# Kernel tuning notes

Measured on AMD Instinct MI355X. Metric: run time of the kernel, lower is better.

Reference implementation:

```python
import jax, jax.numpy as jnp
import numpy as np

MODEL_DIM = 1024
HEAD_DIM = 64
NUM_HEADS = 16
FF_DIM = 4 * MODEL_DIM
ROT_DIM = 32  # max(head_dim // 2, 32)
FUSED = (NUM_HEADS * HEAD_DIM,) * 3 + (FF_DIM,) * 2
B, S = 2, 2048


def rotate_half(x):
    x1, x2 = jnp.split(x, 2, axis=-1)
    return jnp.concatenate([-x2, x1], axis=-1)


def rope_freqs(seq_len, dim=ROT_DIM, max_period=10000.0):
    inv_freq = 1.0 / max_period ** (jnp.arange(0, dim, 2, dtype=jnp.float32) / dim)
    freqs = jnp.arange(seq_len, dtype=jnp.float32)[:, None] * inv_freq[None, :]
    return jnp.concatenate([freqs, freqs], axis=-1)  # [S, dim]


def setup_inputs() -> dict:
    key = jax.random.key(0)
    ks = jax.random.split(key, 10)
    d = MODEL_DIM
    s_in = (sum(FUSED) ** -0.5)
    return {
        "inputs": jax.random.normal(ks[0], (B, S, d), jnp.float32),
        "time_embeds": jax.random.normal(ks[1], (B, 1, d), jnp.float32),
        "ln_w": jnp.ones((d,), jnp.float32),
        "ln_b": jnp.zeros((d,), jnp.float32),
        "cond_w": jax.random.normal(ks[2], (d, 2 * d), jnp.float32) * (d ** -0.5),
        "cond_b": jnp.zeros((2 * d,), jnp.float32),
        "w_in": jax.random.normal(ks[3], (d, sum(FUSED)), jnp.float32) * (d ** -0.5),
        "w_attn": jax.random.normal(ks[4], (NUM_HEADS * HEAD_DIM, d), jnp.float32) * ((NUM_HEADS * HEAD_DIM) ** -0.5),
        "w_ff": jax.random.normal(ks[5], (FF_DIM, d), jnp.float32) * (FF_DIM ** -0.5),
        "b_ff": jnp.zeros((d,), jnp.float32),
    }


def reference(inputs, time_embeds, ln_w, ln_b, cond_w, cond_b, w_in, w_attn, w_ff, b_ff):
    # LayerNorm
    mu = jnp.mean(inputs, axis=-1, keepdims=True)
    var = jnp.mean(jnp.square(inputs - mu), axis=-1, keepdims=True)
    units = (inputs - mu) * jax.lax.rsqrt(var + 1e-5) * ln_w + ln_b

    # FiLM conditioning
    cond = jax.nn.silu(time_embeds) @ cond_w + cond_b  # [B,1,2D]
    scale, bias = jnp.split(cond, 2, axis=-1)
    units = (1.0 + scale) * units + bias

    # Fused projection -> q, k, v, ff, ff_gate
    proj = units @ w_in
    splits = np.cumsum(FUSED)[:-1].tolist()
    q, k, v, ff, ff_gate = jnp.split(proj, splits, axis=-1)

    def split_heads(x):  # [B,S,H*hd] -> [B,H,S,hd]
        return x.reshape(B, S, NUM_HEADS, HEAD_DIM).transpose(0, 2, 1, 3)

    q, k, v = split_heads(q), split_heads(k), split_heads(v)

    # Rotary on first ROT_DIM dims of q, k
    freqs = rope_freqs(S)  # [S, ROT_DIM]
    cos, sin = jnp.cos(freqs), jnp.sin(freqs)

    def rope(x):
        xl, xr = x[..., :ROT_DIM], x[..., ROT_DIM:]
        xl = xl * cos + rotate_half(xl) * sin
        return jnp.concatenate([xl, xr], axis=-1)

    q, k = rope(q), rope(k)

    # Attention (full score matrix, manual softmax, as original)
    score = jnp.einsum("bhsd,bhSd->bhsS", q, k) * (HEAD_DIM ** -0.5)
    weight = jax.nn.softmax(score, axis=-1)
    attn = jnp.einsum("bhsS,bhSd->bhsd", weight, v)
    concat = attn.transpose(0, 2, 1, 3).reshape(B, S, NUM_HEADS * HEAD_DIM)
    attn_out = concat @ w_attn

    # GeGLU FF
    ff_out = (ff * jax.nn.gelu(ff_gate, approximate=True)) @ w_ff + b_ff

    return inputs + attn_out + ff_out
```

## Files before the change

### kernel.cpp

```cpp
#include <hip/hip_runtime.h>
#include <hip/hip_bf16.h>

typedef __attribute__((ext_vector_type(8))) __bf16 bf16x8;
typedef __attribute__((ext_vector_type(4))) float f32x4;
typedef unsigned short u16;
typedef unsigned int u32;

#define DMODEL 1024
#define SLEN   2048
#define NPROJ  11264
#define NFUSE  5120
#define MROWS  4096

__device__ __forceinline__ float b2f(u16 u){ u32 v=((u32)u)<<16; float f; __builtin_memcpy(&f,&v,4); return f; }
__device__ __forceinline__ u16 f2b(float f){ u32 u; __builtin_memcpy(&u,&f,4); u32 r=u+0x7fffu+((u>>16)&1u); return (u16)(r>>16); }
__device__ __forceinline__ float fexp2(float x){ return __builtin_amdgcn_exp2f(x); }

__device__ __forceinline__ void gload16(const void* g, void* l){
  __builtin_amdgcn_global_load_lds((__attribute__((address_space(1))) u32*)g,
                                   (__attribute__((address_space(3))) u32*)l, 16, 0, 0);
}

template<int REMAP>
__global__ __launch_bounds__(256) void k_transpose(const float* __restrict__ src, int N,
                                                   u16* __restrict__ dst, int ldd, int coloff){
  __shared__ float tile[32][33];
  int n0 = blockIdx.x*32, k0 = blockIdx.y*32;
  int tx = threadIdx.x & 31, ty = threadIdx.x >> 5;
  int srccol;
  if (REMAP && (n0 + tx) >= 3072){
    int c = n0 + tx - 3072;
    int q = c >> 5, o = c & 31;
    srccol = (o < 16) ? (3072 + 16*q + o) : (7168 + 16*q + (o-16));
  } else srccol = n0 + tx;
  #pragma unroll
  for (int r=0;r<4;r++)
    tile[ty*4+r][tx] = src[(size_t)(k0+ty*4+r)*N + srccol];
  __syncthreads();
  #pragma unroll
  for (int r=0;r<4;r++){
    int n = ty*4+r;
    dst[(size_t)(n0+n)*ldd + coloff + k0 + tx] = f2b(tile[tx][n]);
  }
}

__global__ __launch_bounds__(256) void k_rope_table(float* __restrict__ tab){
  int idx = blockIdx.x*256 + threadIdx.x;
  if (idx >= SLEN*16) return;
  int s = idx >> 4, i = idx & 15;
  float inv = powf(10000.f, -(float)i/16.f);
  float f = (float)s * inv;
  tab[s*32 + i]      = cosf(f);
  tab[s*32 + 16 + i] = sinf(f);
}

__global__ __launch_bounds__(256) void k_cond(const float* __restrict__ te, const float* __restrict__ cw,
                                              const float* __restrict__ cb, float* __restrict__ cond){
  __shared__ float sl[DMODEL];
  int b = blockIdx.y, t = threadIdx.x;
  for (int i=t;i<DMODEL;i+=256){ float x = te[b*DMODEL+i]; sl[i] = x/(1.f+expf(-x)); }
  __syncthreads();
  int n = blockIdx.x*256 + t;
  float acc = 0.f;
  for (int k=0;k<DMODEL;k++) acc += sl[k]*cw[(size_t)k*2048 + n];
  cond[b*2048+n] = acc + cb[n];
}

__global__ __launch_bounds__(256) void k_ln(const float* __restrict__ x, const float* __restrict__ lw,
                                            const float* __restrict__ lb, const float* __restrict__ cond,
                                            u16* __restrict__ units){
  int row = blockIdx.x; int b = row >> 11;
  int t = threadIdx.x;
  const float4 v = *(const float4*)(x + (size_t)row*DMODEL + t*4);
  float s = v.x+v.y+v.z+v.w;
  float q = v.x*v.x+v.y*v.y+v.z*v.z+v.w*v.w;
  #pragma unroll
  for (int off=32; off; off>>=1){ s += __shfl_xor(s,off); q += __shfl_xor(q,off); }
  __shared__ float red[8];
  int w = t>>6, l = t&63;
  if (l==0){ red[w]=s; red[4+w]=q; }
  __syncthreads();
  float S = red[0]+red[1]+red[2]+red[3];
  float Q = red[4]+red[5]+red[6]+red[7];
  float mu = S*(1.f/1024.f);
  float var = Q*(1.f/1024.f) - mu*mu;
  float rstd = rsqrtf(var + 1e-5f);
  int c0 = t*4;
  u16 o[4];
  const float* vf = (const float*)&v;
  #pragma unroll
  for (int i=0;i<4;i++){
    int c = c0+i;
    float nrm = (vf[i]-mu)*rstd*lw[c] + lb[c];
    float outv = (1.f + cond[b*2048 + c])*nrm + cond[b*2048 + 1024 + c];
    o[i] = f2b(outv);
  }
  u32 p0 = (u32)o[0] | ((u32)o[1]<<16);
  u32 p1 = (u32)o[2] | ((u32)o[3]<<16);
  uint2 pk; pk.x = p0; pk.y = p1;
  *(uint2*)(units + (size_t)row*DMODEL + c0) = pk;
}

template<int BM,int BN,int WM,int WN,int NBUF,int MINW,int EPI>
__global__ __launch_bounds__(WM*WN*64, MINW) void k_gemm_pipe(
    const u16* __restrict__ A, const u16* __restrict__ Bt, int K, int lda, int ldb,
    const float* __restrict__ tab, u16* __restrict__ qh, u16* __restrict__ kh,
    u16* __restrict__ vq, u16* __restrict__ afinal, float* __restrict__ pb)
{
  constexpr int THREADS = WM*WN*64;
  constexpr int MR = BM/WM/16, NR = BN/WN/16;
  constexpr int BUFE = (BM+BN)*32;
  __shared__ __attribute__((aligned(16))) u16 lds[NBUF*BUFE];
  int t = threadIdx.x, w = t>>6, l = t&63;
  int wr = w/WN, wc = w%WN;
  int lane16 = l&15, lg = l>>4;

  int nbx = gridDim.x;
  int wg = blockIdx.y*nbx + blockIdx.x;
  int nwg = nbx*gridDim.y;
  int cpx = nwg>>3;
  int swz = (wg&7)*cpx + (wg>>3);
  int bx = swz % nbx, by = swz / nbx;

  size_t m0 = (size_t)by*BM, n0 = (size_t)bx*BN;
  int koff = (EPI==1) ? blockIdx.z*1280 : 0;
  const u16* Ag = A + m0*lda + koff;
  const u16* Bg = Bt + n0*ldb + koff;

  f32x4 zero = {0.f,0.f,0.f,0.f};
  f32x4 acc[MR][NR];
  #pragma unroll
  for (int i=0;i<MR;i++)
    #pragma unroll
    for (int j=0;j<NR;j++) acc[i][j] = zero;

  const int ntiles = K/32;

  auto STAGE = [&](int tt, int buf){
    int k0 = tt*32;
    char* Ad = (char*)lds + (size_t)buf*(BUFE*2);
    char* Bd = Ad + BM*64;
    #pragma unroll
    for (int i=0;i<2;i++){
      int s = i*THREADS + t;
      int r = s>>2, g = s&3;
      int src = (g ^ ((r>>1)&3))*8;
      gload16(Ag + (size_t)r*lda + k0 + src, Ad + (i*THREADS + w*64)*16);
      gload16(Bg + (size_t)r*ldb + k0 + src, Bd + (i*THREADS + w*64)*16);
    }
  };

  #pragma unroll
  for (int p=0;p<NBUF-1;p++) STAGE(p, p);

  int cur = 0;
  for (int kt=0; kt<ntiles; ++kt){
    int rem = ntiles-1-kt;
    if (rem>=1)      asm volatile("s_waitcnt vmcnt(4)" ::: "memory");
    else             asm volatile("s_waitcnt vmcnt(0)" ::: "memory");
    __builtin_amdgcn_s_barrier();
    const u16* As = lds + (size_t)cur*BUFE;
    const u16* Bs = As + BM*32;
    bf16x8 af[MR], bf[NR];
    #pragma unroll
    for (int i=0;i<MR;i++){
      int r = wr*(MR*16) + i*16 + lane16;
      int g = lg ^ ((r>>1)&3);
      af[i] = *(const bf16x8*)(As + r*32 + g*8);
    }
    #pragma unroll
    for (int j=0;j<NR;j++){
      int r = wc*(NR*16) + j*16 + lane16;
      int g = lg ^ ((r>>1)&3);
      bf[j] = *(const bf16x8*)(Bs + r*32 + g*8);
    }
    int st = kt + NBUF-1;
    if (st < ntiles) STAGE(st, (cur==0)?(NBUF-1):(cur-1));
    __builtin_amdgcn_s_setprio(1);
    #pragma unroll
    for (int i=0;i<MR;i++)
      #pragma unroll
      for (int j=0;j<NR;j++)
        acc[i][j] = __builtin_amdgcn_mfma_f32_16x16x32_bf16(af[i], bf[j], acc[i][j], 0,0,0);
    __builtin_amdgcn_s_setprio(0);
    __builtin_amdgcn_sched_barrier(0);
    cur = (cur+1==NBUF)?0:(cur+1);
  }

  if constexpr (EPI==0){
    int region = (n0 < 3072) ? (int)(n0>>10) : 3;
    if (region<=1){
      u16* dst = (region==0)? qh : kh;
      float sc = (region==0)? 0.125f*1.44269504f : 1.0f;
      int h = (int)((n0 & 1023)>>6) + wc;
      int d = lane16;
      #pragma unroll
      for (int i=0;i<MR;i++){
        #pragma unroll
        for (int r=0;r<4;r++){
          int row = (int)m0 + wr*(MR*16) + i*16 + lg*4 + r;
          int bb = row>>11, s = row&2047;
          float cs = tab[s*32+d], sn = tab[s*32+16+d];
          float x0 = acc[i][0][r], x1 = acc[i][1][r];
          size_t base = ((size_t)(bb*16+h)*SLEN + s)*64;
          dst[base+d]    = f2b((x0*cs - x1*sn)*sc);
          dst[base+16+d] = f2b((x1*cs + x0*sn)*sc);
          dst[base+32+d] = f2b(acc[i][2][r]*sc);
          dst[base+48+d] = f2b(acc[i][3][r]*sc);
        }
      }
    } else if (region==2){
      #pragma unroll
      for (int i=0;i<MR;i++)
        #pragma unroll
        for (int j=0;j<NR;j++){
          int cv = (int)(n0-2048) + wc*64 + j*16 + lane16;
          #pragma unroll
          for (int r=0;r<4;r++){
            int row = (int)m0 + wr*(MR*16) + i*16 + lg*4 + r;
            vq[(size_t)row*DMODEL + cv] = f2b(acc[i][j][r]);
          }
        }
    } else {
      int fbase = (int)((n0-3072)>>1) + wc*32 + lane16;
      #pragma unroll
      for (int i=0;i<MR;i++)
        #pragma unroll
        for (int p=0;p<2;p++){
          int col = 1024 + fbase + p*16;
          #pragma unroll
          for (int r=0;r<4;r++){
            int row = (int)m0 + wr*(MR*16) + i*16 + lg*4 + r;
            float fv = acc[i][2*p][r];
            float gv = acc[i][2*p+1][r];
            float tz = 0.7978845608f*(gv + 0.044715f*gv*gv*gv);
            float th = 1.f - 2.f/(__expf(2.f*tz)+1.f);
            afinal[(size_t)row*NFUSE + col] = f2b(fv * 0.5f*gv*(1.f+th));
          }
        }
    }
  } else {
    float* pbs = pb + (size_t)blockIdx.z*MROWS*DMODEL;
    #pragma unroll
    for (int i=0;i<MR;i++)
      #pragma unroll
      for (int j=0;j<NR;j++){
        int col = (int)n0 + wc*(NR*16) + j*16 + lane16;
        #pragma unroll
        for (int r=0;r<4;r++){
          int row = (int)m0 + wr*(MR*16) + i*16 + lg*4 + r;
          pbs[(size_t)row*DMODEL + col] = acc[i][j][r];
        }
      }
  }
}

__global__ __launch_bounds__(256) void k_reduce(const float* __restrict__ pb, const float* __restrict__ resid,
                                                const float* __restrict__ bias, float* __restrict__ out){
  size_t i4 = ((size_t)blockIdx.x*256 + threadIdx.x)*4;
  float4 a0 = *(const float4*)(pb + i4);
  float4 a1 = *(const float4*)(pb + (size_t)MROWS*DMODEL + i4);
  float4 a2 = *(const float4*)(pb + (size_t)2*MROWS*DMODEL + i4);
  float4 a3 = *(const float4*)(pb + (size_t)3*MROWS*DMODEL + i4);
  float4 rv = *(const float4*)(resid + i4);
  float4 bv = *(const float4*)(bias + (i4 & 1023));
  float4 o;
  o.x = a0.x+a1.x+a2.x+a3.x+rv.x+bv.x;
  o.y = a0.y+a1.y+a2.y+a3.y+rv.y+bv.y;
  o.z = a0.z+a1.z+a2.z+a3.z+rv.z+bv.z;
  o.w = a0.w+a1.w+a2.w+a3.w+rv.w+bv.w;
  *(float4*)(out + i4) = o;
}

__global__ __launch_bounds__(256) void k_vtrans(const u16* __restrict__ vq, u16* __restrict__ vt){
  int b = blockIdx.z, h = blockIdx.y, s0 = blockIdx.x*64;
  int t = threadIdx.x;
  __shared__ u16 vt_lds[64][72];
  int sl = t>>2, quad = t&3;
  const u16* prow = vq + (size_t)(b*SLEN + s0 + sl)*DMODEL + h*64;
  #pragma unroll
  for (int i=0;i<16;i++){
    int d = quad*16+i;
    vt_lds[d][sl] = prow[d];
  }
  __syncthreads();
  int d = t>>2, sg = t&3;
  size_t base = ((size_t)(b*16+h)*64 + d)*SLEN + s0 + sg*16;
  #pragma unroll
  for (int i=0;i<16;i++)
    vt[base + i] = vt_lds[d][sg*16+i];
}

#define M0SHIFT 20.0f
__global__ __launch_bounds__(256,3) void k_attn(const u16* __restrict__ qh, const u16* __restrict__ kh,
                                                const u16* __restrict__ vt,
                                                float* __restrict__ op, float* __restrict__ lsum){
  __shared__ __attribute__((aligned(16))) u16 Klds[2][64*64];
  __shared__ __attribute__((aligned(16))) u16 Vlds[2][64*64];
  __shared__ __attribute__((aligned(16))) u16 Plds[4][32*72];
  int p = (blockIdx.z*16 + blockIdx.y)*16 + blockIdx.x;
  int c = p&7, k = p>>3;
  int hb = c + 8*(k&3);
  int rem = k>>2;
  int split = rem>>4, qx = rem&15;
  int b = hb>>4, h = hb&15, q0 = qx*128;
  int kvbase = split*1024;
  int t = threadIdx.x, w = t>>6, l = t&63;
  int lane16 = l&15, lg = l>>4;
  size_t hoff = (size_t)hb*SLEN*64;
  const u16* Qb = qh + hoff + (size_t)(q0 + w*32)*64;
  const u16* Kb = kh + hoff;
  const u16* Vb = vt + hoff;
  bf16x8 qf[2][2];
  #pragma unroll
  for (int mi=0;mi<2;mi++)
    #pragma unroll
    for (int ks=0;ks<2;ks++)
      qf[mi][ks] = *(const bf16x8*)(Qb + (size_t)(mi*16+lane16)*64 + ks*32 + lg*8);
  bf16x8 ones;
  #pragma unroll
  for (int i=0;i<8;i++) ones[i] = (__bf16)1.0f;
  f32x4 zero = {0.f,0.f,0.f,0.f};
  f32x4 acc[2][4];
  f32x4 lacc[2];
  #pragma unroll
  for (int mi=0;mi<2;mi++){
    lacc[mi] = zero;
    #pragma unroll
    for (int n=0;n<4;n++) acc[mi][n] = zero;
  }

  auto STAGE = [&](int buf, int kv0){
    #pragma unroll
    for (int r=0;r<2;r++){
      int cc = r*256 + t;
      int row = cc>>3;
      int g = (cc&7) ^ (row&7);
      gload16(Kb + (size_t)(kv0+row)*64 + g*8, (char*)Klds[buf] + r*4096 + w*1024);
      gload16(Vb + (size_t)row*SLEN + kv0 + g*8, (char*)Vlds[buf] + r*4096 + w*1024);
    }
  };

  STAGE(0, kvbase);
  __syncthreads();

  for (int tile=0; tile<16; ++tile){
    int cur = tile & 1;
    if (tile+1 < 16) STAGE(cur^1, kvbase + (tile+1)*64);
    f32x4 sf[2][4];
    #pragma unroll
    for (int mi=0;mi<2;mi++)
      #pragma unroll
      for (int n=0;n<4;n++) sf[mi][n] = zero;
    __builtin_amdgcn_s_setprio(1);
    #pragma unroll
    for (int n=0;n<4;n++){
      #pragma unroll
      for (int ks=0;ks<2;ks++){
        int rk = n*16 + lane16;
        int g = (ks*4 + lg) ^ (rk&7);
        bf16x8 kf = *(const bf16x8*)(Klds[cur] + rk*64 + g*8);
        sf[0][n] = __builtin_amdgcn_mfma_f32_16x16x32_bf16(qf[0][ks], kf, sf[0][n], 0,0,0);
        sf[1][n] = __builtin_amdgcn_mfma_f32_16x16x32_bf16(qf[1][ks], kf, sf[1][n], 0,0,0);
      }
    }
    __builtin_amdgcn_s_setprio(0);
    #pragma unroll
    for (int mi=0;mi<2;mi++)
      #pragma unroll
      for (int jr=0;jr<4;jr++)
        #pragma unroll
        for (int n=0;n<4;n++){
          float pv = fexp2(sf[mi][n][jr] - M0SHIFT);
          u32 u; __builtin_memcpy(&u,&pv,4);
          Plds[w][(mi*16 + lg*4 + jr)*72 + n*16 + lane16] = (u16)(u>>16);
        }
    __builtin_amdgcn_s_setprio(1);
    #pragma unroll
    for (int ks=0;ks<2;ks++){
      bf16x8 vf[4];
      #pragma unroll
      for (int n=0;n<4;n++){
        int rv = n*16 + lane16;
        int g = (ks*4 + lg) ^ (rv&7);
        vf[n] = *(const bf16x8*)(Vlds[cur] + rv*64 + g*8);
      }
      #pragma unroll
      for (int mi=0;mi<2;mi++){
        bf16x8 pa = *(const bf16x8*)(&Plds[w][(mi*16 + lane16)*72 + ks*32 + lg*8]);
        #pragma unroll
        for (int n=0;n<4;n++)
          acc[mi][n] = __builtin_amdgcn_mfma_f32_16x16x32_bf16(pa, vf[n], acc[mi][n], 0,0,0);
        lacc[mi] = __builtin_amdgcn_mfma_f32_16x16x32_bf16(pa, ones, lacc[mi], 0,0,0);
      }
    }
    __builtin_amdgcn_s_setprio(0);
    __syncthreads();
  }
  float* ops = op + (size_t)split*MROWS*DMODEL;
  #pragma unroll
  for (int mi=0;mi<2;mi++)
    #pragma unroll
    for (int n=0;n<4;n++)
      #pragma unroll
      for (int jr=0;jr<4;jr++){
        int srow = q0 + w*32 + mi*16 + lg*4 + jr;
        size_t r = (size_t)b*SLEN + srow;
        ops[r*DMODEL + h*64 + n*16 + lane16] = acc[mi][n][jr];
      }
  if (lane16==0){
    #pragma unroll
    for (int mi=0;mi<2;mi++)
      #pragma unroll
      for (int jr=0;jr<4;jr++){
        int srow = q0 + w*32 + mi*16 + lg*4 + jr;
        size_t r = (size_t)b*SLEN + srow;
        lsum[((size_t)split*MROWS + r)*16 + h] = lacc[mi][jr];
      }
  }
}

__global__ __launch_bounds__(256) void k_attn_combine(const float* __restrict__ op,
                                                      const float* __restrict__ lsum,
                                                      u16* __restrict__ afinal){
  size_t i4 = ((size_t)blockIdx.x*256 + threadIdx.x)*4;
  int r = (int)(i4>>10), col = (int)(i4&1023), h = col>>6;
  float l0 = lsum[(size_t)r*16+h];
  float l1 = lsum[((size_t)MROWS + r)*16 + h];
  float inv = 1.f/(l0 + l1);
  float4 o0 = *(const float4*)(op + i4);
  float4 o1 = *(const float4*)(op + (size_t)MROWS*DMODEL + i4);
  union { u16 o[4]; uint2 v; } res;
  res.o[0] = f2b((o0.x + o1.x)*inv);
  res.o[1] = f2b((o0.y + o1.y)*inv);
  res.o[2] = f2b((o0.z + o1.z)*inv);
  res.o[3] = f2b((o0.w + o1.w)*inv);
  *(uint2*)(afinal + (size_t)r*NFUSE + col) = res.v;
}

extern "C" void kernel_launch(void* const* d_in, const int* in_sizes, int n_in,
                              void* d_out, int out_size, void* d_ws, size_t ws_size,
                              hipStream_t stream) {
  const float* inputs = (const float*)d_in[0];
  const float* te     = (const float*)d_in[1];
  const float* ln_w   = (const float*)d_in[2];
  const float* ln_b   = (const float*)d_in[3];
  const float* cond_w = (const float*)d_in[4];
  const float* cond_b = (const float*)d_in[5];
  const float* w_in   = (const float*)d_in[6];
  const float* w_attn = (const float*)d_in[7];
  const float* w_ff   = (const float*)d_in[8];
  const float* b_ff   = (const float*)d_in[9];
  float* out = (float*)d_out;

  char* ws = (char*)d_ws;
  size_t off = 0;
  auto alloc = [&](size_t n)->char*{ char* p = ws + off; off += (n + 255) & ~(size_t)255; return p; };
  u16*  w_inT    = (u16*)alloc((size_t)NPROJ*DMODEL*2);
  u16*  w_fusedT = (u16*)alloc((size_t)DMODEL*NFUSE*2);
  u16*  units    = (u16*)alloc((size_t)MROWS*DMODEL*2);
  u16*  qh       = (u16*)alloc((size_t)MROWS*DMODEL*2);
  u16*  kh       = (u16*)alloc((size_t)MROWS*DMODEL*2);
  u16*  vq       = (u16*)alloc((size_t)MROWS*DMODEL*2);
  u16*  vT       = (u16*)alloc((size_t)MROWS*DMODEL*2);
  u16*  afinal   = (u16*)alloc((size_t)MROWS*NFUSE*2);
  float* pb      = (float*)alloc((size_t)4*MROWS*DMODEL*4);
  float* lsum    = (float*)alloc((size_t)2*MROWS*16*4);
  float* cond    = (float*)alloc(2*2048*4);
  float* ropetab = (float*)alloc((size_t)SLEN*32*4);
  float* op      = pb;
  (void)ws_size; (void)in_sizes; (void)n_in; (void)out_size;

  k_transpose<1><<<dim3(NPROJ/32, DMODEL/32), 256, 0, stream>>>(w_in, NPROJ, w_inT, DMODEL, 0);
  k_transpose<0><<<dim3(DMODEL/32, DMODEL/32), 256, 0, stream>>>(w_attn, DMODEL, w_fusedT, NFUSE, 0);
  k_transpose<0><<<dim3(DMODEL/32, 4096/32), 256, 0, stream>>>(w_ff, DMODEL, w_fusedT, NFUSE, DMODEL);
  k_rope_table<<<128, 256, 0, stream>>>(ropetab);
  k_cond<<<dim3(8,2), 256, 0, stream>>>(te, cond_w, cond_b, cond);
  k_ln<<<MROWS, 256, 0, stream>>>(inputs, ln_w, ln_b, cond, units);
  k_gemm_pipe<256,256,2,4,3,2,0><<<dim3(NPROJ/256, MROWS/256), 512, 0, stream>>>(
      units, w_inT, DMODEL, DMODEL, DMODEL, ropetab, qh, kh, vq, afinal, nullptr);
  k_vtrans<<<dim3(SLEN/64, 16, 2), 256, 0, stream>>>(vq, vT);
  k_attn<<<dim3(16, 16, 4), 256, 0, stream>>>(qh, kh, vT, op, lsum);
  k_attn_combine<<<dim3(MROWS*DMODEL/1024), 256, 0, stream>>>(op, lsum, afinal);
  k_gemm_pipe<128,128,2,2,3,3,1><<<dim3(DMODEL/128, MROWS/128, 4), 256, 0, stream>>>(
      afinal, w_fusedT, 1280, NFUSE, NFUSE, nullptr, nullptr, nullptr, nullptr, nullptr, pb);
  k_reduce<<<dim3(MROWS*DMODEL/1024), 256, 0, stream>>>(pb, inputs, b_ff, out);
}
```

Before: 325.1 us.

## Add dedicated 8-wave projection GEMM with BK=64 and interleaved quarter-tile staging

Replaces the generic pipelined GEMM used for the fused input projection with a specialized 256x256 kernel that uses K-tiles of 64, double-buffered LDS with XOR swizzle, and splits each K-step into four MFMA quarters interleaved with partial global-to-LDS loads and barriers. The aim is to overlap loads with MFMA more finely and halve the number of K iterations, reducing barrier and LDS read overhead. It uses 128KB of LDS and many barriers per step, and the launch bound of 2 may not be achievable given LDS size, limiting occupancy. The epilogue (rope, v, GeGLU) is moved unchanged into the new kernel.

```diff
diff --git a/kernel.cpp b/kernel.cpp
--- a/kernel.cpp
+++ b/kernel.cpp
@@ -20,6 +20,8 @@
   __builtin_amdgcn_global_load_lds((__attribute__((address_space(1))) u32*)g,
                                    (__attribute__((address_space(3))) u32*)l, 16, 0, 0);
 }
+
+#define BARR asm volatile("s_barrier" ::: "memory")
 
 template<int REMAP>
 __global__ __launch_bounds__(256) void k_transpose(const float* __restrict__ src, int N,
@@ -101,6 +103,179 @@
   *(uint2*)(units + (size_t)row*DMODEL + c0) = pk;
 }
 
+__global__ __launch_bounds__(512,2) void k_gemm8_proj(
+    const u16* __restrict__ A, const u16* __restrict__ Bt, const float* __restrict__ tab,
+    u16* __restrict__ qh, u16* __restrict__ kh, u16* __restrict__ vq, u16* __restrict__ afinal)
+{
+  __shared__ __attribute__((aligned(16))) u16 lds[65536];
+  int t = threadIdx.x, w = t>>6, l = t&63;
+  int wr = w>>2, wc = w&3;
+  int lane16 = l&15, lg = l>>4;
+
+  int nbx = gridDim.x;
+  int wg = blockIdx.y*nbx + blockIdx.x;
+  int nwg = nbx*gridDim.y;
+  int cpx = nwg>>3;
+  int swz = (wg&7)*cpx + (wg>>3);
+  int bx = swz % nbx, by = swz / nbx;
+
+  size_t m0 = (size_t)by*256, n0 = (size_t)bx*256;
+  const u16* Ag = A + m0*DMODEL;
+  const u16* Bg = Bt + n0*DMODEL;
+
+  f32x4 zero = {0.f,0.f,0.f,0.f};
+  f32x4 acc[8][4];
+  #pragma unroll
+  for (int i=0;i<8;i++)
+    #pragma unroll
+    for (int j=0;j<4;j++) acc[i][j] = zero;
+
+  bf16x8 a[8][2], bv[4][2];
+
+  auto STAGEA = [&](int u, int h){
+    const u16* src = Ag + (size_t)(h*128)*DMODEL + u*64;
+    char* dst = (char*)lds + ((u&1)<<16) + (h<<14);
+    #pragma unroll
+    for (int i=0;i<2;i++){
+      int cid = i*512 + t;
+      int r = cid>>3, s2 = cid&7;
+      gload16(src + (size_t)r*DMODEL + ((s2 ^ (r&7))<<3), dst + ((i*512 + w*64)<<4));
+    }
+  };
+  auto STAGEB = [&](int u, int h){
+    const u16* src = Bg + (size_t)(h*128)*DMODEL + u*64;
+    char* dst = (char*)lds + ((u&1)<<16) + 32768 + (h<<14);
+    #pragma unroll
+    for (int i=0;i<2;i++){
+      int cid = i*512 + t;
+      int r = cid>>3, s2 = cid&7;
+      gload16(src + (size_t)r*DMODEL + ((s2 ^ (r&7))<<3), dst + ((i*512 + w*64)<<4));
+    }
+  };
+  auto LDA4 = [&](int u, int fi0){
+    const char* base = (const char*)lds + ((u&1)<<16) + (wr<<14);
+    #pragma unroll
+    for (int i=0;i<4;i++){
+      int r = (fi0+i)*16 + lane16;
+      #pragma unroll
+      for (int kk=0;kk<2;kk++){
+        int c = kk*4 + lg;
+        a[fi0+i][kk] = *(const bf16x8*)(base + r*128 + ((c ^ (r&7))<<4));
+      }
+    }
+  };
+  auto LDB2 = [&](int u, int fj0){
+    const char* base = (const char*)lds + ((u&1)<<16) + 32768 + ((wc>>1)<<14);
+    #pragma unroll
+    for (int j=0;j<2;j++){
+      int r = (wc&1)*64 + (fj0+j)*16 + lane16;
+      #pragma unroll
+      for (int kk=0;kk<2;kk++){
+        int c = kk*4 + lg;
+        bv[fj0+j][kk] = *(const bf16x8*)(base + r*128 + ((c ^ (r&7))<<4));
+      }
+    }
+  };
+  auto MMQ = [&](int I0, int J0){
+    #pragma unroll
+    for (int i=0;i<4;i++)
+      #pragma unroll
+      for (int j=0;j<2;j++)
+        #pragma unroll
+        for (int kk=0;kk<2;kk++)
+          acc[I0+i][J0+j] = __builtin_amdgcn_mfma_f32_16x16x32_bf16(
+              a[I0+i][kk], bv[J0+j][kk], acc[I0+i][J0+j], 0,0,0);
+  };
+
+  const int T = DMODEL/64;
+  STAGEA(0,0); STAGEA(0,1); STAGEB(0,0); STAGEB(0,1); STAGEA(1,0); STAGEA(1,1);
+  asm volatile("s_waitcnt vmcnt(4)" ::: "memory");
+  BARR;
+
+  for (int u=0; u<T; ++u){
+    LDA4(u,0); LDB2(u,0);
+    if (u+1<T) STAGEB(u+1,0);
+    BARR;
+    __builtin_amdgcn_s_setprio(1);
+    MMQ(0,0);
+    __builtin_amdgcn_s_setprio(0);
+    BARR;
+    LDA4(u,4);
+    if (u+1<T) STAGEB(u+1,1);
+    BARR;
+    __builtin_amdgcn_s_setprio(1);
+    MMQ(4,0);
+    __builtin_amdgcn_s_setprio(0);
+    BARR;
+    LDB2(u,2);
+    if (u+2<T) STAGEA(u+2,0);
+    BARR;
+    __builtin_amdgcn_s_setprio(1);
+    MMQ(0,2);
+    __builtin_amdgcn_s_setprio(0);
+    BARR;
+    if (u+2<T) STAGEA(u+2,1);
+    BARR;
+    __builtin_amdgcn_s_setprio(1);
+    MMQ(4,2);
+    __builtin_amdgcn_s_setprio(0);
+    asm volatile("s_waitcnt vmcnt(4)" ::: "memory");
+    BARR;
+  }
+
+  int region = (n0 < 3072) ? (int)(n0>>10) : 3;
+  if (region<=1){
+    u16* dst = (region==0)? qh : kh;
+    float sc = (region==0)? 0.125f*1.44269504f : 1.0f;
+    int h = (int)((n0 & 1023)>>6) + wc;
+    int d = lane16;
+    #pragma unroll
+    for (int i=0;i<8;i++){
+      #pragma unroll
+      for (int r=0;r<4;r++){
+        int row = (int)m0 + wr*128 + i*16 + lg*4 + r;
+        int bb = row>>11, s = row&2047;
+        float cs = tab[s*32+d], sn = tab[s*32+16+d];
+        float x0 = acc[i][0][r], x1 = acc[i][1][r];
+        size_t base = ((size_t)(bb*16+h)*SLEN + s)*64;
+        dst[base+d]    = f2b((x0*cs - x1*sn)*sc);
+        dst[base+16+d] = f2b((x1*cs + x0*sn)*sc);
+        dst[base+32+d] = f2b(acc[i][2][r]*sc);
+        dst[base+48+d] = f2b(acc[i][3][r]*sc);
+      }
+    }
+  } else if (region==2){
+    #pragma unroll
+    for (int i=0;i<8;i++)
+      #pragma unroll
+      for (int j=0;j<4;j++){
+        int cv = (int)(n0-2048) + wc*64 + j*16 + lane16;
+        #pragma unroll
+        for (int r=0;r<4;r++){
+          int row = (int)m0 + wr*128 + i*16 + lg*4 + r;
+          vq[(size_t)row*DMODEL + cv] = f2b(acc[i][j][r]);
+        }
+      }
+  } else {
+    int fbase = (int)((n0-3072)>>1) + wc*32 + lane16;
+    #pragma unroll
+    for (int i=0;i<8;i++)
+      #pragma unroll
+      for (int p=0;p<2;p++){
+        int col = 1024 + fbase + p*16;
+        #pragma unroll
+        for (int r=0;r<4;r++){
+          int row = (int)m0 + wr*128 + i*16 + lg*4 + r;
+          float fv = acc[i][2*p][r];
+          float gv = acc[i][2*p+1][r];
+          float tz = 0.7978845608f*(gv + 0.044715f*gv*gv*gv);
+          float th = 1.f - 2.f/(__expf(2.f*tz)+1.f);
+          afinal[(size_t)row*NFUSE + col] = f2b(fv * 0.5f*gv*(1.f+th));
+        }
+      }
+  }
+}
+
 template<int BM,int BN,int WM,int WN,int NBUF,int MINW,int EPI>
 __global__ __launch_bounds__(WM*WN*64, MINW) void k_gemm_pipe(
     const u16* __restrict__ A, const u16* __restrict__ Bt, int K, int lda, int ldb,
@@ -187,59 +362,7 @@
     cur = (cur+1==NBUF)?0:(cur+1);
   }
 
-  if constexpr (EPI==0){
-    int region = (n0 < 3072) ? (int)(n0>>10) : 3;
-    if (region<=1){
-      u16* dst = (region==0)? qh : kh;
-      float sc = (region==0)? 0.125f*1.44269504f : 1.0f;
-      int h = (int)((n0 & 1023)>>6) + wc;
-      int d = lane16;
-      #pragma unroll
-      for (int i=0;i<MR;i++){
-        #pragma unroll
-        for (int r=0;r<4;r++){
-          int row = (int)m0 + wr*(MR*16) + i*16 + lg*4 + r;
-          int bb = row>>11, s = row&2047;
-          float cs = tab[s*32+d], sn = tab[s*32+16+d];
-          float x0 = acc[i][0][r], x1 = acc[i][1][r];
-          size_t base = ((size_t)(bb*16+h)*SLEN + s)*64;
-          dst[base+d]    = f2b((x0*cs - x1*sn)*sc);
-          dst[base+16+d] = f2b((x1*cs + x0*sn)*sc);
-          dst[base+32+d] = f2b(acc[i][2][r]*sc);
-          dst[base+48+d] = f2b(acc[i][3][r]*sc);
-        }
-      }
-    } else if (region==2){
-      #pragma unroll
-      for (int i=0;i<MR;i++)
-        #pragma unroll
-        for (int j=0;j<NR;j++){
-          int cv = (int)(n0-2048) + wc*64 + j*16 + lane16;
-          #pragma unroll
-          for (int r=0;r<4;r++){
-            int row = (int)m0 + wr*(MR*16) + i*16 + lg*4 + r;
-            vq[(size_t)row*DMODEL + cv] = f2b(acc[i][j][r]);
-          }
-        }
-    } else {
-      int fbase = (int)((n0-3072)>>1) + wc*32 + lane16;
-      #pragma unroll
-      for (int i=0;i<MR;i++)
-        #pragma unroll
-        for (int p=0;p<2;p++){
-          int col = 1024 + fbase + p*16;
-          #pragma unroll
-          for (int r=0;r<4;r++){
-            int row = (int)m0 + wr*(MR*16) + i*16 + lg*4 + r;
-            float fv = acc[i][2*p][r];
-            float gv = acc[i][2*p+1][r];
-            float tz = 0.7978845608f*(gv + 0.044715f*gv*gv*gv);
-            float th = 1.f - 2.f/(__expf(2.f*tz)+1.f);
-            afinal[(size_t)row*NFUSE + col] = f2b(fv * 0.5f*gv*(1.f+th));
-          }
-        }
-    }
-  } else {
+  if constexpr (EPI==1){
     float* pbs = pb + (size_t)blockIdx.z*MROWS*DMODEL;
     #pragma unroll
     for (int i=0;i<MR;i++)
@@ -477,8 +600,7 @@
   k_rope_table<<<128, 256, 0, stream>>>(ropetab);
   k_cond<<<dim3(8,2), 256, 0, stream>>>(te, cond_w, cond_b, cond);
   k_ln<<<MROWS, 256, 0, stream>>>(inputs, ln_w, ln_b, cond, units);
-  k_gemm_pipe<256,256,2,4,3,2,0><<<dim3(NPROJ/256, MROWS/256), 512, 0, stream>>>(
-      units, w_inT, DMODEL, DMODEL, DMODEL, ropetab, qh, kh, vq, afinal, nullptr);
+  k_gemm8_proj<<<dim3(NPROJ/256, MROWS/256), 512, 0, stream>>>(units, w_inT, ropetab, qh, kh, vq, afinal);
   k_vtrans<<<dim3(SLEN/64, 16, 2), 256, 0, stream>>>(vq, vT);
   k_attn<<<dim3(16, 16, 4), 256, 0, stream>>>(qh, kh, vT, op, lsum);
   k_attn_combine<<<dim3(MROWS*DMODEL/1024), 256, 0, stream>>>(op, lsum, afinal);
```

Result: no change. 321.8 us (-1.0%).
